# Performance work log

Measured on AMD Instinct MI355X. Metric: run time of the kernel, lower is better.

## Reference

```python
import jax, jax.numpy as jnp
import numpy as np

IMG = 40  # imgSize hard-coded in FFTNet


def _fft_layer(z, w):
    # z: complex64 [B, inC, H, W]; w: float32 [inC, outC, H, W, 2]
    # torch.fft(..., 2, normalized=True) == 2D FFT with 'ortho' norm over last two dims
    F = jnp.fft.fft2(z, norm='ortho')
    wc = jax.lax.complex(w[..., 0], w[..., 1])
    # dft_conv: per-frequency complex multiply then sum over input channels
    # (Karatsuba trick in the original == plain complex multiply)
    mixed = jnp.einsum('bihw,iohw->bohw', F, wc)
    return jnp.fft.ifft2(mixed, norm='ortho')


def _crelu(z):
    # F.relu applied to the stacked [..., 2] real/imag tensor => relu each part
    return jax.lax.complex(jax.nn.relu(z.real), jax.nn.relu(z.imag))


def _fftnet(x, ws):
    # x: [B, 1, H, W] real; stacked with zeros -> complex input
    z = x.astype(jnp.complex64)
    for w in ws[:-1]:
        z = _crelu(_fft_layer(z, w))
    z = _fft_layer(z, ws[-1])
    return z.real  # x[..., 0]


def setup_inputs() -> dict:
    key = jax.random.key(0)
    ks = jax.random.split(key, 7)
    B = 256
    x = jax.random.normal(ks[0], (B, 1, IMG, IMG), dtype=jnp.float32)

    def make_w(k, i, o):
        # xavier_normal_ on torch shape (1, i, o, H, W, 2):
        # fan_in = i * (o*H*W*2), fan_out = 1 * (o*H*W*2)
        recept = o * IMG * IMG * 2
        std = float(np.sqrt(2.0 / (i * recept + recept)))
        return jax.random.normal(k, (i, o, IMG, IMG, 2), dtype=jnp.float32) * std

    chans = [(1, 40), (40, 40), (40, 40), (40, 40), (40, 40), (40, 1)]
    inp = {'x': x}
    for n, (k, (i, o)) in enumerate(zip(ks[1:], chans), start=1):
        inp[f'w{n}'] = make_w(k, i, o)
    return inp


def reference(x, w1, w2, w3, w4, w5, w6):
    return _fftnet(x, (w1, w2, w3, w4, w5, w6))
```

## Files before the change

kernel.cpp:

```cpp
#include <hip/hip_runtime.h>
#include <math.h>

#define NPIX 1600
#define NIMG 40
#define SW   40
#define PSZ  (48 * SW)

#define RST 322
#define OST 482

typedef __bf16 bf16x8 __attribute__((ext_vector_type(8)));
typedef float  f32x4  __attribute__((ext_vector_type(4)));
#define MFMA __builtin_amdgcn_mfma_f32_16x16x32_bf16

__device__ __forceinline__ unsigned short bits16(__bf16 x) {
    return __builtin_bit_cast(unsigned short, x);
}

__device__ __forceinline__ void cfma(float2& acc, float ax, float ay, float bx, float by) {
    acc.x = fmaf(ax, bx, fmaf(-ay, by, acc.x));
    acc.y = fmaf(ax, by, fmaf( ay, bx, acc.y));
}

__global__ void init_dtab(unsigned short* __restrict__ Dtab) {
    int idx = blockIdx.x * 256 + threadIdx.x;
    if (idx >= 2304) return;
    int rec = idx >> 6, lane = idx & 63;
    int p = rec % 6, t = (rec / 6) % 3, kc = rec / 18;
    unsigned short out[8];
    for (int j = 0; j < 8; ++j) {
        int k = kc * 32 + (lane >> 4) * 8 + j;
        int n = t * 16 + (lane & 15);
        float val = 0.0f;
        if (k < 40 && n < 40) {
            float ang = 6.28318530717958647692f * (float)((k * n) % 40) / 40.0f;
            float dr, di, s, c;
            sincosf(ang, &s, &c);
            dr = c; di = s;
            float base = (p < 2) ? dr : (p < 4) ? di : -di;
            __bf16 hi = (__bf16)base;
            if ((p & 1) == 0) val = (float)hi;
            else              val = (float)(__bf16)(base - (float)hi);
        }
        out[j] = __builtin_bit_cast(unsigned short, (__bf16)val);
    }
    unsigned short* dst = Dtab + (size_t)rec * 512 + lane * 8;
    for (int j = 0; j < 8; ++j) dst[j] = out[j];
}

template<bool REAL_IN, bool RELU, bool REAL_OUT>
__global__ __launch_bounds__(256) void fft2_kernel(const void* __restrict__ inv,
                                                   void* __restrict__ outv,
                                                   int dir)
{
    const int img = blockIdx.x;
    const int tid = threadIdx.x;
    __shared__ float2 A[NPIX];
    __shared__ float2 T[NPIX];
    __shared__ float2 D[NPIX];
    __shared__ float2 tw[NIMG];

    if (tid < NIMG) {
        float ang = (float)dir * 6.28318530717958647692f * (float)tid / 40.0f;
        float s, c;
        sincosf(ang, &s, &c);
        tw[tid] = make_float2(c, s);
    }
    if (REAL_IN) {
        const float* in = (const float*)inv + (size_t)img * NPIX;
        for (int idx = tid; idx < NPIX; idx += 256)
            A[idx] = make_float2(in[idx], 0.0f);
    } else {
        const float2* in = (const float2*)inv + (size_t)img * NPIX;
        for (int idx = tid; idx < NPIX; idx += 256)
            A[idx] = in[idx];
    }
    __syncthreads();
    for (int idx = tid; idx < NPIX; idx += 256) {
        int a = idx / NIMG, b = idx - a * NIMG;
        D[idx] = tw[(a * b) % NIMG];
    }
    __syncthreads();

    for (int idx = tid; idx < NPIX; idx += 256) {
        int h = idx / NIMG, v = idx - h * NIMG;
        float2 s = make_float2(0.0f, 0.0f);
        const float2* Arow = &A[h * NIMG];
        #pragma unroll
        for (int w = 0; w < NIMG; ++w) {
            float2 a = Arow[w];
            float2 d = D[w * NIMG + v];
            s.x += a.x * d.x - a.y * d.y;
            s.y += a.x * d.y + a.y * d.x;
        }
        T[idx] = s;
    }
    __syncthreads();

    for (int idx = tid; idx < NPIX; idx += 256) {
        int u = idx / NIMG, v = idx - u * NIMG;
        float2 s = make_float2(0.0f, 0.0f);
        const float2* Du = &D[u * NIMG];
        #pragma unroll
        for (int h = 0; h < NIMG; ++h) {
            float2 t = T[h * NIMG + v];
            float2 d = Du[h];
            s.x += t.x * d.x - t.y * d.y;
            s.y += t.x * d.y + t.y * d.x;
        }
        s.x *= 0.025f;
        s.y *= 0.025f;
        if (RELU) { s.x = fmaxf(s.x, 0.0f); s.y = fmaxf(s.y, 0.0f); }
        if (REAL_OUT) {
            ((float*)outv)[(size_t)img * NPIX + idx] = s.x;
        } else {
            ((float2*)outv)[(size_t)img * NPIX + idx] = s;
        }
    }
}

__device__ __forceinline__ void mac_row(f32x4& aR, f32x4& aI,
    bf16x8 xrh, bf16x8 xrl, bf16x8 xih, bf16x8 xil,
    bf16x8 drh, bf16x8 drl, bf16x8 dih, bf16x8 dil, bf16x8 dnh, bf16x8 dnl)
{
    aR = MFMA(xrh, drh, aR, 0, 0, 0);
    aR = MFMA(xrl, drh, aR, 0, 0, 0);
    aR = MFMA(xrh, drl, aR, 0, 0, 0);
    aR = MFMA(xih, dnh, aR, 0, 0, 0);
    aR = MFMA(xil, dnh, aR, 0, 0, 0);
    aR = MFMA(xih, dnl, aR, 0, 0, 0);
    aI = MFMA(xrh, dih, aI, 0, 0, 0);
    aI = MFMA(xrl, dih, aI, 0, 0, 0);
    aI = MFMA(xrh, dil, aI, 0, 0, 0);
    aI = MFMA(xih, drh, aI, 0, 0, 0);
    aI = MFMA(xil, drh, aI, 0, 0, 0);
    aI = MFMA(xih, drl, aI, 0, 0, 0);
}

__device__ __forceinline__ void mac_col(f32x4& aR, f32x4& aI,
    bf16x8 drh, bf16x8 drl, bf16x8 dih, bf16x8 dil, bf16x8 dnh, bf16x8 dnl,
    bf16x8 trh, bf16x8 trl, bf16x8 tih, bf16x8 til)
{
    aR = MFMA(drh, trh, aR, 0, 0, 0);
    aR = MFMA(drl, trh, aR, 0, 0, 0);
    aR = MFMA(drh, trl, aR, 0, 0, 0);
    aR = MFMA(dnh, tih, aR, 0, 0, 0);
    aR = MFMA(dnl, tih, aR, 0, 0, 0);
    aR = MFMA(dnh, til, aR, 0, 0, 0);
    aI = MFMA(drh, tih, aI, 0, 0, 0);
    aI = MFMA(drl, tih, aI, 0, 0, 0);
    aI = MFMA(drh, til, aI, 0, 0, 0);
    aI = MFMA(dih, trh, aI, 0, 0, 0);
    aI = MFMA(dil, trh, aI, 0, 0, 0);
    aI = MFMA(dih, trl, aI, 0, 0, 0);
}

__device__ __forceinline__ void mac_mix(f32x4& aR, f32x4& aI,
    bf16x8 frh, bf16x8 frl, bf16x8 fih, bf16x8 fil, bf16x8 fnih, bf16x8 fnil,
    bf16x8 wrh, bf16x8 wrl, bf16x8 wih, bf16x8 wil)
{
    aR = MFMA(frh,  wrh, aR, 0, 0, 0);
    aR = MFMA(frl,  wrh, aR, 0, 0, 0);
    aR = MFMA(frh,  wrl, aR, 0, 0, 0);
    aR = MFMA(fnih, wih, aR, 0, 0, 0);
    aR = MFMA(fnil, wih, aR, 0, 0, 0);
    aR = MFMA(fnih, wil, aR, 0, 0, 0);
    aI = MFMA(frh,  wih, aI, 0, 0, 0);
    aI = MFMA(frl,  wih, aI, 0, 0, 0);
    aI = MFMA(frh,  wil, aI, 0, 0, 0);
    aI = MFMA(fih,  wrh, aI, 0, 0, 0);
    aI = MFMA(fil,  wrh, aI, 0, 0, 0);
    aI = MFMA(fih,  wrl, aI, 0, 0, 0);
}

__global__ __launch_bounds__(512, 2) void mix_mfma_kernel(const float2* __restrict__ F,
                                                          const float2* __restrict__ W,
                                                          float2* __restrict__ M)
{
    __shared__ alignas(16) char smem[102912];
    float2* raw  = (float2*)smem;
    float2* outt = (float2*)(smem + 41216);
    float2* lw   = (float2*)smem;

    const int tid  = threadIdx.x;
    const int w    = tid >> 6;
    const int lane = tid & 63;
    const int q    = lane >> 4;
    const int m    = lane & 15;
    const int fw   = blockIdx.x >> 3;
    const int bg   = blockIdx.x & 7;
    const int f0   = fw * 8;
    const int fsub = w;

    f32x4 pf[5];
    #pragma unroll
    for (int k = 0; k < 5; ++k) {
        int c = tid + (k << 9);
        int r = c >> 2, sub = c & 3;
        int b = r / 40, i = r - b * 40;
        const f32x4* g = (const f32x4*)(F + ((size_t)((bg * 32 + b) * 40 + i) * NPIX + f0));
        pf[k] = __builtin_nontemporal_load(g + sub);
    }

    #pragma unroll
    for (int k = 0; k < 13; ++k) {
        int c = tid + (k << 9);
        if (c < 6400) {
            int r = c >> 2, sub = c & 3;
            const f32x4* g = (const f32x4*)(W + ((size_t)r * NPIX + f0));
            *(f32x4*)&lw[r * 8 + sub * 2] = g[sub];
        }
    }
    __syncthreads();

    bf16x8 wt[2][3][4];
    #pragma unroll
    for (int kc = 0; kc < 2; ++kc) {
        #pragma unroll
        for (int nt = 0; nt < 3; ++nt) {
            bf16x8 wrh = (bf16x8){}, wrl = (bf16x8){};
            bf16x8 wih = (bf16x8){}, wil = (bf16x8){};
            const int o = nt * 16 + m;
            const bool have = ((kc == 0) || (q == 0)) && (o < 40);
            if (have) {
                #pragma unroll
                for (int j = 0; j < 8; ++j) {
                    int i = kc * 32 + q * 8 + j;
                    float2 v = lw[(i * 40 + o) * 8 + fsub];
                    __bf16 h1 = (__bf16)v.x;
                    wrh[j] = h1; wrl[j] = (__bf16)(v.x - (float)h1);
                    __bf16 h2 = (__bf16)v.y;
                    wih[j] = h2; wil[j] = (__bf16)(v.y - (float)h2);
                }
            }
            wt[kc][nt][0] = wrh; wt[kc][nt][1] = wrl;
            wt[kc][nt][2] = wih; wt[kc][nt][3] = wil;
        }
    }
    __syncthreads();

    #pragma unroll
    for (int bt = 0; bt < 2; ++bt) {
        const int btile = bg * 2 + bt;

        #pragma unroll
        for (int k = 0; k < 5; ++k) {
            int c = tid + (k << 9);
            int r = c >> 2, sub = c & 3;
            int b = r / 40, i = r - b * 40;
            *(f32x4*)&raw[b * RST + i * 8 + sub * 2] = pf[k];
        }
        __syncthreads();

        if (bt == 0) {
            #pragma unroll
            for (int k = 0; k < 5; ++k) {
                int c = tid + (k << 9);
                int r = c >> 2, sub = c & 3;
                int b = r / 40, i = r - b * 40;
                const f32x4* g = (const f32x4*)(F + ((size_t)(((bg * 2 + 1) * 16 + b) * 40 + i) * NPIX + f0));
                pf[k] = __builtin_nontemporal_load(g + sub);
            }
        }

        f32x4 accR[3], accI[3];
        #pragma unroll
        for (int nt = 0; nt < 3; ++nt) {
            accR[nt] = (f32x4){0.f, 0.f, 0.f, 0.f};
            accI[nt] = (f32x4){0.f, 0.f, 0.f, 0.f};
        }

        #pragma unroll
        for (int kc = 0; kc < 2; ++kc) {
            const bool have = (kc == 0) || (q == 0);
            float re[8], im[8];
            #pragma unroll
            for (int j = 0; j < 8; ++j) {
                int i = kc * 32 + q * 8 + j;
                if (have) {
                    float2 v = raw[m * RST + i * 8 + fsub];
                    re[j] = v.x; im[j] = v.y;
                } else { re[j] = 0.f; im[j] = 0.f; }
            }
            bf16x8 frh, frl, fih, fil, fnih, fnil;
            #pragma unroll
            for (int j = 0; j < 8; ++j) {
                __bf16 h1 = (__bf16)re[j];
                frh[j] = h1;
                float lo = re[j] - (float)h1;
                frl[j] = (__bf16)lo;
                __bf16 h2 = (__bf16)im[j];
                fih[j] = h2;
                float lo2 = im[j] - (float)h2;
                fil[j] = (__bf16)lo2;
                fnih[j] = (__bf16)(-(float)h2);
                fnil[j] = (__bf16)(-lo2);
            }
            #pragma unroll
            for (int nt = 0; nt < 3; ++nt)
                mac_mix(accR[nt], accI[nt], frh, frl, fih, fil, fnih, fnil,
                        wt[kc][nt][0], wt[kc][nt][1], wt[kc][nt][2], wt[kc][nt][3]);
        }

        #pragma unroll
        for (int nt = 0; nt < 3; ++nt)
            #pragma unroll
            for (int g2 = 0; g2 < 4; ++g2)
                outt[(q * 4 + g2) * OST + (nt * 16 + m) * 10 + fsub] =
                    make_float2(accR[nt][g2], accI[nt][g2]);
        __syncthreads();

        #pragma unroll
        for (int k = 0; k < 5; ++k) {
            int c = tid + (k << 9);
            int r = c >> 2, sub = c & 3;
            int b = r / 40, o = r - b * 40;
            f32x4 v = *(const f32x4*)&outt[b * OST + o * 10 + sub * 2];
            f32x4* g = (f32x4*)(M + ((size_t)((btile * 16 + b) * 40 + o) * NPIX + f0));
            __builtin_nontemporal_store(v, g + sub);
        }
    }
}

__global__ __launch_bounds__(64) void fused_mfma_kernel(const float2* __restrict__ in,
                                                        float2* __restrict__ outg,
                                                        const unsigned short* __restrict__ Dtab)
{
    __shared__ unsigned short Pl[4 * PSZ];

    const int lane = threadIdx.x;
    const int q = lane >> 4;
    const int m = lane & 15;

    bf16x8 dreg[36];
    #pragma unroll
    for (int r = 0; r < 36; ++r)
        dreg[r] = ((const bf16x8*)Dtab)[r * 64 + lane];

    #pragma unroll 1
    for (int ii = 0; ii < 5; ++ii) {
        const size_t img  = (size_t)blockIdx.x + (size_t)ii * 2048;
        const size_t base = img * NPIX;

        {
            const float4* src = (const float4*)(in + base);
            #pragma unroll
            for (int c = 0; c < 13; ++c) {
                int p = c * 64 + lane;
                if (p < 800) {
                    float4 v = src[p];
                    int h = p / 20, w2 = (p - h * 20) * 2;
                    int o = h * SW + w2;
                    __bf16 rh0 = (__bf16)v.x, ih0 = (__bf16)v.y;
                    __bf16 rh1 = (__bf16)v.z, ih1 = (__bf16)v.w;
                    ushort2 s0, s1, s2, s3;
                    s0.x = bits16(rh0); s0.y = bits16(rh1);
                    s1.x = bits16((__bf16)(v.x - (float)rh0));
                    s1.y = bits16((__bf16)(v.z - (float)rh1));
                    s2.x = bits16(ih0); s2.y = bits16(ih1);
                    s3.x = bits16((__bf16)(v.y - (float)ih0));
                    s3.y = bits16((__bf16)(v.w - (float)ih1));
                    *(ushort2*)&Pl[0 * PSZ + o] = s0;
                    *(ushort2*)&Pl[1 * PSZ + o] = s1;
                    *(ushort2*)&Pl[2 * PSZ + o] = s2;
                    *(ushort2*)&Pl[3 * PSZ + o] = s3;
                }
            }
            #pragma unroll
            for (int c = 0; c < 5; ++c) {
                int idx = c * 64 + lane;
                int pl = idx / 80, rem = idx - pl * 80;
                int r = 40 + rem / 10, c4 = (rem - (rem / 10) * 10) * 4;
                *(ushort4*)&Pl[pl * PSZ + r * SW + c4] = make_ushort4(0, 0, 0, 0);
            }
        }
        __syncthreads();

        f32x4 accR[3][3], accI[3][3];

        #pragma unroll
        for (int rep = 0; rep < 2; ++rep) {
            const int IP = rep ? 4 : 2;
            const int IN = rep ? 2 : 4;

            #pragma unroll
            for (int a = 0; a < 3; ++a)
                #pragma unroll
                for (int b = 0; b < 3; ++b) {
                    accR[a][b] = (f32x4){0.f, 0.f, 0.f, 0.f};
                    accI[a][b] = (f32x4){0.f, 0.f, 0.f, 0.f};
                }

            #pragma unroll
            for (int kc = 0; kc < 2; ++kc) {
                bf16x8 arh[3], arl[3], aih[3], ail[3];
                const bool have = (kc == 0) || (q == 0);
                #pragma unroll
                for (int mt = 0; mt < 3; ++mt) {
                    if (have) {
                        int o = (mt * 16 + m) * SW + kc * 32 + q * 8;
                        arh[mt] = *(const bf16x8*)&Pl[0 * PSZ + o];
                        arl[mt] = *(const bf16x8*)&Pl[1 * PSZ + o];
                        aih[mt] = *(const bf16x8*)&Pl[2 * PSZ + o];
                        ail[mt] = *(const bf16x8*)&Pl[3 * PSZ + o];
                    } else {
                        arh[mt] = (bf16x8){}; arl[mt] = (bf16x8){};
                        aih[mt] = (bf16x8){}; ail[mt] = (bf16x8){};
                    }
                }
                __builtin_amdgcn_s_setprio(1);
                #pragma unroll
                for (int nt = 0; nt < 3; ++nt) {
                    const int rb = (kc * 3 + nt) * 6;
                    #pragma unroll
                    for (int mt = 0; mt < 3; ++mt)
                        mac_row(accR[mt][nt], accI[mt][nt],
                                arh[mt], arl[mt], aih[mt], ail[mt],
                                dreg[rb + 0], dreg[rb + 1],
                                dreg[rb + IP], dreg[rb + IP + 1],
                                dreg[rb + IN], dreg[rb + IN + 1]);
                }
                __builtin_amdgcn_s_setprio(0);
            }
            __syncthreads();

            #pragma unroll
            for (int mt = 0; mt < 3; ++mt) {
                int hb = mt * 16 + q * 4;
                if (hb < 40) {
                    #pragma unroll
                    for (int nt = 0; nt < 3; ++nt) {
                        int v = nt * 16 + m;
                        f32x4 r = accR[mt][nt], i2 = accI[mt][nt];
                        ushort4 srh, srl, sih, sil;
                        unsigned short* prh = (unsigned short*)&srh;
                        unsigned short* prl = (unsigned short*)&srl;
                        unsigned short* pih = (unsigned short*)&sih;
                        unsigned short* pil = (unsigned short*)&sil;
                        #pragma unroll
                        for (int g = 0; g < 4; ++g) {
                            __bf16 h1 = (__bf16)r[g];
                            prh[g] = bits16(h1);
                            prl[g] = bits16((__bf16)(r[g] - (float)h1));
                            __bf16 h2 = (__bf16)i2[g];
                            pih[g] = bits16(h2);
                            pil[g] = bits16((__bf16)(i2[g] - (float)h2));
                        }
                        int o = v * SW + hb;
                        *(ushort4*)&Pl[0 * PSZ + o] = srh;
                        *(ushort4*)&Pl[1 * PSZ + o] = srl;
                        *(ushort4*)&Pl[2 * PSZ + o] = sih;
                        *(ushort4*)&Pl[3 * PSZ + o] = sil;
                    }
                }
            }
            __syncthreads();

            #pragma unroll
            for (int a = 0; a < 3; ++a)
                #pragma unroll
                for (int b = 0; b < 3; ++b) {
                    accR[a][b] = (f32x4){0.f, 0.f, 0.f, 0.f};
                    accI[a][b] = (f32x4){0.f, 0.f, 0.f, 0.f};
                }

            #pragma unroll
            for (int kc = 0; kc < 2; ++kc) {
                bf16x8 trh[3], trl[3], tih[3], til[3];
                const bool have = (kc == 0) || (q == 0);
                #pragma unroll
                for (int nt = 0; nt < 3; ++nt) {
                    trh[nt] = (bf16x8){}; trl[nt] = (bf16x8){};
                    tih[nt] = (bf16x8){}; til[nt] = (bf16x8){};
                    if (have) {
                        int o = (nt * 16 + m) * SW + kc * 32 + q * 8;
                        trh[nt] = *(const bf16x8*)&Pl[0 * PSZ + o];
                        trl[nt] = *(const bf16x8*)&Pl[1 * PSZ + o];
                        tih[nt] = *(const bf16x8*)&Pl[2 * PSZ + o];
                        til[nt] = *(const bf16x8*)&Pl[3 * PSZ + o];
                    }
                }
                __builtin_amdgcn_s_setprio(1);
                #pragma unroll
                for (int mt = 0; mt < 3; ++mt) {
                    const int rb = (kc * 3 + mt) * 6;
                    #pragma unroll
                    for (int nt = 0; nt < 3; ++nt)
                        mac_col(accR[mt][nt], accI[mt][nt],
                                dreg[rb + 0], dreg[rb + 1],
                                dreg[rb + IP], dreg[rb + IP + 1],
                                dreg[rb + IN], dreg[rb + IN + 1],
                                trh[nt], trl[nt], tih[nt], til[nt]);
                }
                __builtin_amdgcn_s_setprio(0);
            }
            __syncthreads();

            if (rep == 0) {
                #pragma unroll
                for (int mt = 0; mt < 3; ++mt) {
                    int u0 = mt * 16 + q * 4;
                    if (u0 < 40) {
                        #pragma unroll
                        for (int nt = 0; nt < 3; ++nt) {
                            int v = nt * 16 + m;
                            if (v < 40) {
                                f32x4 r = accR[mt][nt], i2 = accI[mt][nt];
                                ushort4 srh, srl, sih, sil;
                                unsigned short* prh = (unsigned short*)&srh;
                                unsigned short* prl = (unsigned short*)&srl;
                                unsigned short* pih = (unsigned short*)&sih;
                                unsigned short* pil = (unsigned short*)&sil;
                                #pragma unroll
                                for (int g = 0; g < 4; ++g) {
                                    float xr = fmaxf(r[g] * 0.025f, 0.f);
                                    float xi = fmaxf(i2[g] * 0.025f, 0.f);
                                    __bf16 h1 = (__bf16)xr;
                                    prh[g] = bits16(h1);
                                    prl[g] = bits16((__bf16)(xr - (float)h1));
                                    __bf16 h2 = (__bf16)xi;
                                    pih[g] = bits16(h2);
                                    pil[g] = bits16((__bf16)(xi - (float)h2));
                                }
                                int o = v * SW + u0;
                                *(ushort4*)&Pl[0 * PSZ + o] = srh;
                                *(ushort4*)&Pl[1 * PSZ + o] = srl;
                                *(ushort4*)&Pl[2 * PSZ + o] = sih;
                                *(ushort4*)&Pl[3 * PSZ + o] = sil;
                            }
                        }
                    }
                }
                __syncthreads();
            } else {
                float2* dst = outg + base;
                #pragma unroll
                for (int mt = 0; mt < 3; ++mt) {
                    int u0 = mt * 16 + q * 4;
                    if (u0 < 40) {
                        #pragma unroll
                        for (int nt = 0; nt < 3; ++nt) {
                            int v = nt * 16 + m;
                            if (v < 40) {
                                f32x4 r = accR[mt][nt], i2 = accI[mt][nt];
                                float4 s0, s1;
                                s0.x = r[0] * 0.025f; s0.y = i2[0] * 0.025f;
                                s0.z = r[1] * 0.025f; s0.w = i2[1] * 0.025f;
                                s1.x = r[2] * 0.025f; s1.y = i2[2] * 0.025f;
                                s1.z = r[3] * 0.025f; s1.w = i2[3] * 0.025f;
                                *(float4*)&dst[v * NIMG + u0]     = s0;
                                *(float4*)&dst[v * NIMG + u0 + 2] = s1;
                            }
                        }
                    }
                }
            }
        }
        __syncthreads();
    }
}

template<int INC, int OUTC, int BT, int OT>
__global__ __launch_bounds__(256) void mix_kernel(const float2* __restrict__ F,
                                                  const float2* __restrict__ W,
                                                  float2* __restrict__ M)
{
    const int tid = threadIdx.x;
    const int lane = tid & 63;
    const int wv = tid >> 6;
    const int f = (blockIdx.x % 25) * 64 + lane;
    const int bg = (blockIdx.x / 25) * 4 + wv;
    const int b0 = bg * BT;

    #pragma unroll
    for (int o0 = 0; o0 < OUTC; o0 += OT) {
        float2 acc[BT][OT];
        #pragma unroll
        for (int t = 0; t < BT; ++t)
            #pragma unroll
            for (int o = 0; o < OT; ++o)
                acc[t][o] = make_float2(0.0f, 0.0f);

        for (int i = 0; i < INC; ++i) {
            float2 fv[BT];
            #pragma unroll
            for (int t = 0; t < BT; ++t)
                fv[t] = F[((size_t)(b0 + t) * INC + i) * NPIX + f];
            float2 wr[OT];
            #pragma unroll
            for (int o = 0; o < OT; ++o)
                wr[o] = W[((size_t)i * OUTC + (o0 + o)) * NPIX + f];
            #pragma unroll
            for (int t = 0; t < BT; ++t)
                #pragma unroll
                for (int o = 0; o < OT; ++o)
                    cfma(acc[t][o], fv[t].x, fv[t].y, wr[o].x, wr[o].y);
        }
        #pragma unroll
        for (int t = 0; t < BT; ++t)
            #pragma unroll
            for (int o = 0; o < OT; ++o)
                M[((size_t)(b0 + t) * OUTC + (o0 + o)) * NPIX + f] = acc[t][o];
    }
}

extern "C" void kernel_launch(void* const* d_in, const int* in_sizes, int n_in,
                              void* d_out, int out_size, void* d_ws, size_t ws_size,
                              hipStream_t stream)
{
    const float* x = (const float*)d_in[0];
    const float2* w[6];
    for (int i = 0; i < 6; ++i) w[i] = (const float2*)d_in[1 + i];
    float* out = (float*)d_out;

    const size_t bufBytes = (size_t)256 * 40 * NPIX * sizeof(float2);
    float2* A = (float2*)d_ws;
    float2* B = (float2*)((char*)d_ws + bufBytes);
    unsigned short* Dtab = (unsigned short*)((char*)d_ws + 2 * bufBytes);

    const int FUSEGRID = 2048;
    const int MIXBLK = 25 * (256 / 4) / 4;

    init_dtab<<<9, 256, 0, stream>>>(Dtab);

    fft2_kernel<true, false, false><<<256, 256, 0, stream>>>(x, A, -1);

    mix_kernel<1, 40, 4, 10><<<MIXBLK, 256, 0, stream>>>(A, w[0], B);
    fused_mfma_kernel<<<FUSEGRID, 64, 0, stream>>>(B, A, Dtab);

    for (int l = 1; l <= 4; ++l) {
        mix_mfma_kernel<<<1600, 512, 0, stream>>>(A, w[l], B);
        fused_mfma_kernel<<<FUSEGRID, 64, 0, stream>>>(B, A, Dtab);
    }

    mix_kernel<40, 1, 4, 1><<<MIXBLK, 256, 0, stream>>>(A, w[5], B);
    fft2_kernel<false, false, true><<<256, 256, 0, stream>>>(B, out, +1);
}
```

Baseline: 1.552 ms.

## Negate activation operands on the fly to shrink DFT register table and raise occupancy

The fused FFT kernel previously kept 36 bf16x8 DFT-matrix fragments in registers, including pre-negated imaginary parts, for the forward and inverse transforms. It now keeps only 24 fragments and gets the sign flips by XOR-negating the activation fragments per tile, with a direction-dependent choice of which operand to negate. The freed registers allow a launch bound of 3 waves per SIMD, and the grid grows from 2048 to 2560 blocks with 4 images each instead of 5. Loads and MFMAs are also interleaved per tile rather than batched, which adds some VALU sign-flip work and may reduce load/MFMA overlap.

Result: slower. 2.040 ms (+31.4%).

```diff
diff --git a/kernel.cpp b/kernel.cpp
--- a/kernel.cpp
+++ b/kernel.cpp
@@ -11,10 +11,17 @@
 
 typedef __bf16 bf16x8 __attribute__((ext_vector_type(8)));
 typedef float  f32x4  __attribute__((ext_vector_type(4)));
+typedef unsigned int u32x4v __attribute__((ext_vector_type(4)));
 #define MFMA __builtin_amdgcn_mfma_f32_16x16x32_bf16
 
 __device__ __forceinline__ unsigned short bits16(__bf16 x) {
     return __builtin_bit_cast(unsigned short, x);
+}
+
+__device__ __forceinline__ bf16x8 bneg(bf16x8 x) {
+    u32x4v u = __builtin_bit_cast(u32x4v, x);
+    u = u ^ (u32x4v){0x80008000u, 0x80008000u, 0x80008000u, 0x80008000u};
+    return __builtin_bit_cast(bf16x8, u);
 }
 
 __device__ __forceinline__ void cfma(float2& acc, float ax, float ay, float bx, float by) {
@@ -119,40 +126,42 @@
     }
 }
 
-__device__ __forceinline__ void mac_row(f32x4& aR, f32x4& aI,
+__device__ __forceinline__ void mac_cplx(f32x4& aR, f32x4& aI,
     bf16x8 xrh, bf16x8 xrl, bf16x8 xih, bf16x8 xil,
-    bf16x8 drh, bf16x8 drl, bf16x8 dih, bf16x8 dil, bf16x8 dnh, bf16x8 dnl)
+    bf16x8 ph,  bf16x8 pl,  bf16x8 qh,  bf16x8 ql,
+    bf16x8 drh, bf16x8 drl, bf16x8 dih, bf16x8 dil)
 {
     aR = MFMA(xrh, drh, aR, 0, 0, 0);
     aR = MFMA(xrl, drh, aR, 0, 0, 0);
     aR = MFMA(xrh, drl, aR, 0, 0, 0);
-    aR = MFMA(xih, dnh, aR, 0, 0, 0);
-    aR = MFMA(xil, dnh, aR, 0, 0, 0);
-    aR = MFMA(xih, dnl, aR, 0, 0, 0);
-    aI = MFMA(xrh, dih, aI, 0, 0, 0);
-    aI = MFMA(xrl, dih, aI, 0, 0, 0);
-    aI = MFMA(xrh, dil, aI, 0, 0, 0);
+    aR = MFMA(ph,  dih, aR, 0, 0, 0);
+    aR = MFMA(pl,  dih, aR, 0, 0, 0);
+    aR = MFMA(ph,  dil, aR, 0, 0, 0);
+    aI = MFMA(qh,  dih, aI, 0, 0, 0);
+    aI = MFMA(ql,  dih, aI, 0, 0, 0);
+    aI = MFMA(qh,  dil, aI, 0, 0, 0);
     aI = MFMA(xih, drh, aI, 0, 0, 0);
     aI = MFMA(xil, drh, aI, 0, 0, 0);
     aI = MFMA(xih, drl, aI, 0, 0, 0);
 }
 
-__device__ __forceinline__ void mac_col(f32x4& aR, f32x4& aI,
-    bf16x8 drh, bf16x8 drl, bf16x8 dih, bf16x8 dil, bf16x8 dnh, bf16x8 dnl,
-    bf16x8 trh, bf16x8 trl, bf16x8 tih, bf16x8 til)
+__device__ __forceinline__ void mac_cplx_col(f32x4& aR, f32x4& aI,
+    bf16x8 drh, bf16x8 drl, bf16x8 dih, bf16x8 dil,
+    bf16x8 trh, bf16x8 trl, bf16x8 tih, bf16x8 til,
+    bf16x8 ph,  bf16x8 pl,  bf16x8 qh,  bf16x8 ql)
 {
     aR = MFMA(drh, trh, aR, 0, 0, 0);
     aR = MFMA(drl, trh, aR, 0, 0, 0);
     aR = MFMA(drh, trl, aR, 0, 0, 0);
-    aR = MFMA(dnh, tih, aR, 0, 0, 0);
-    aR = MFMA(dnl, tih, aR, 0, 0, 0);
-    aR = MFMA(dnh, til, aR, 0, 0, 0);
+    aR = MFMA(dih, ph,  aR, 0, 0, 0);
+    aR = MFMA(dil, ph,  aR, 0, 0, 0);
+    aR = MFMA(dih, pl,  aR, 0, 0, 0);
+    aI = MFMA(dih, qh,  aI, 0, 0, 0);
+    aI = MFMA(dil, qh,  aI, 0, 0, 0);
+    aI = MFMA(dih, ql,  aI, 0, 0, 0);
     aI = MFMA(drh, tih, aI, 0, 0, 0);
     aI = MFMA(drl, tih, aI, 0, 0, 0);
     aI = MFMA(drh, til, aI, 0, 0, 0);
-    aI = MFMA(dih, trh, aI, 0, 0, 0);
-    aI = MFMA(dil, trh, aI, 0, 0, 0);
-    aI = MFMA(dih, trl, aI, 0, 0, 0);
 }
 
 __device__ __forceinline__ void mac_mix(f32x4& aR, f32x4& aI,
@@ -322,9 +331,9 @@
     }
 }
 
-__global__ __launch_bounds__(64) void fused_mfma_kernel(const float2* __restrict__ in,
-                                                        float2* __restrict__ outg,
-                                                        const unsigned short* __restrict__ Dtab)
+__global__ __launch_bounds__(64, 3) void fused_mfma_kernel(const float2* __restrict__ in,
+                                                           float2* __restrict__ outg,
+                                                           const unsigned short* __restrict__ Dtab)
 {
     __shared__ unsigned short Pl[4 * PSZ];
 
@@ -332,14 +341,16 @@
     const int q = lane >> 4;
     const int m = lane & 15;
 
-    bf16x8 dreg[36];
+    bf16x8 dreg[24];
     #pragma unroll
-    for (int r = 0; r < 36; ++r)
-        dreg[r] = ((const bf16x8*)Dtab)[r * 64 + lane];
+    for (int t = 0; t < 6; ++t)
+        #pragma unroll
+        for (int p = 0; p < 4; ++p)
+            dreg[t * 4 + p] = ((const bf16x8*)Dtab)[((size_t)t * 6 + p) * 64 + lane];
 
     #pragma unroll 1
-    for (int ii = 0; ii < 5; ++ii) {
-        const size_t img  = (size_t)blockIdx.x + (size_t)ii * 2048;
+    for (int ii = 0; ii < 4; ++ii) {
+        const size_t img  = (size_t)blockIdx.x + (size_t)ii * 2560;
         const size_t base = img * NPIX;
 
         {
@@ -380,8 +391,6 @@
 
         #pragma unroll
         for (int rep = 0; rep < 2; ++rep) {
-            const int IP = rep ? 4 : 2;
-            const int IN = rep ? 2 : 4;
 
             #pragma unroll
             for (int a = 0; a < 3; ++a)
@@ -393,34 +402,33 @@
 
             #pragma unroll
             for (int kc = 0; kc < 2; ++kc) {
-                bf16x8 arh[3], arl[3], aih[3], ail[3];
                 const bool have = (kc == 0) || (q == 0);
                 #pragma unroll
                 for (int mt = 0; mt < 3; ++mt) {
+                    bf16x8 xrh, xrl, xih, xil;
                     if (have) {
                         int o = (mt * 16 + m) * SW + kc * 32 + q * 8;
-                        arh[mt] = *(const bf16x8*)&Pl[0 * PSZ + o];
-                        arl[mt] = *(const bf16x8*)&Pl[1 * PSZ + o];
-                        aih[mt] = *(const bf16x8*)&Pl[2 * PSZ + o];
-                        ail[mt] = *(const bf16x8*)&Pl[3 * PSZ + o];
+                        xrh = *(const bf16x8*)&Pl[0 * PSZ + o];
+                        xrl = *(const bf16x8*)&Pl[1 * PSZ + o];
+                        xih = *(const bf16x8*)&Pl[2 * PSZ + o];
+                        xil = *(const bf16x8*)&Pl[3 * PSZ + o];
                     } else {
-                        arh[mt] = (bf16x8){}; arl[mt] = (bf16x8){};
-                        aih[mt] = (bf16x8){}; ail[mt] = (bf16x8){};
+                        xrh = (bf16x8){}; xrl = (bf16x8){};
+                        xih = (bf16x8){}; xil = (bf16x8){};
                     }
-                }
-                __builtin_amdgcn_s_setprio(1);
-                #pragma unroll
-                for (int nt = 0; nt < 3; ++nt) {
-                    const int rb = (kc * 3 + nt) * 6;
+                    bf16x8 ph, pl2, qh, ql;
+                    if (rep == 0) { ph = bneg(xih); pl2 = bneg(xil); qh = xrh; ql = xrl; }
+                    else          { ph = xih;       pl2 = xil;       qh = bneg(xrh); ql = bneg(xrl); }
+                    __builtin_amdgcn_s_setprio(1);
                     #pragma unroll
-                    for (int mt = 0; mt < 3; ++mt)
-                        mac_row(accR[mt][nt], accI[mt][nt],
-                                arh[mt], arl[mt], aih[mt], ail[mt],
-                                dreg[rb + 0], dreg[rb + 1],
-                                dreg[rb + IP], dreg[rb + IP + 1],
-                                dreg[rb + IN], dreg[rb + IN + 1]);
-                }
-                __builtin_amdgcn_s_setprio(0);
+                    for (int nt = 0; nt < 3; ++nt) {
+                        const int rb = (kc * 3 + nt) * 4;
+                        mac_cplx(accR[mt][nt], accI[mt][nt],
+                                 xrh, xrl, xih, xil, ph, pl2, qh, ql,
+                                 dreg[rb + 0], dreg[rb + 1], dreg[rb + 2], dreg[rb + 3]);
+                    }
+                    __builtin_amdgcn_s_setprio(0);
+                }
             }
             __syncthreads();
 
@@ -466,33 +474,33 @@
 
             #pragma unroll
             for (int kc = 0; kc < 2; ++kc) {
-                bf16x8 trh[3], trl[3], tih[3], til[3];
                 const bool have = (kc == 0) || (q == 0);
                 #pragma unroll
                 for (int nt = 0; nt < 3; ++nt) {
-                    trh[nt] = (bf16x8){}; trl[nt] = (bf16x8){};
-                    tih[nt] = (bf16x8){}; til[nt] = (bf16x8){};
+                    bf16x8 trh, trl, tih, til;
                     if (have) {
                         int o = (nt * 16 + m) * SW + kc * 32 + q * 8;
-                        trh[nt] = *(const bf16x8*)&Pl[0 * PSZ + o];
-                        trl[nt] = *(const bf16x8*)&Pl[1 * PSZ + o];
-                        tih[nt] = *(const bf16x8*)&Pl[2 * PSZ + o];
-                        til[nt] = *(const bf16x8*)&Pl[3 * PSZ + o];
+                        trh = *(const bf16x8*)&Pl[0 * PSZ + o];
+                        trl = *(const bf16x8*)&Pl[1 * PSZ + o];
+                        tih = *(const bf16x8*)&Pl[2 * PSZ + o];
+                        til = *(const bf16x8*)&Pl[3 * PSZ + o];
+                    } else {
+                        trh = (bf16x8){}; trl = (bf16x8){};
+                        tih = (bf16x8){}; til = (bf16x8){};
                     }
-                }
-                __builtin_amdgcn_s_setprio(1);
-                #pragma unroll
-                for (int mt = 0; mt < 3; ++mt) {
-                    const int rb = (kc * 3 + mt) * 6;
+                    bf16x8 ph, pl2, qh, ql;
+                    if (rep == 0) { ph = bneg(tih); pl2 = bneg(til); qh = trh; ql = trl; }
+                    else          { ph = tih;       pl2 = til;       qh = bneg(trh); ql = bneg(trl); }
+                    __builtin_amdgcn_s_setprio(1);
                     #pragma unroll
-                    for (int nt = 0; nt < 3; ++nt)
-                        mac_col(accR[mt][nt], accI[mt][nt],
-                                dreg[rb + 0], dreg[rb + 1],
-                                dreg[rb + IP], dreg[rb + IP + 1],
-                                dreg[rb + IN], dreg[rb + IN + 1],
-                                trh[nt], trl[nt], tih[nt], til[nt]);
-                }
-                __builtin_amdgcn_s_setprio(0);
+                    for (int mt = 0; mt < 3; ++mt) {
+                        const int rb = (kc * 3 + mt) * 4;
+                        mac_cplx_col(accR[mt][nt], accI[mt][nt],
+                                     dreg[rb + 0], dreg[rb + 1], dreg[rb + 2], dreg[rb + 3],
+                                     trh, trl, tih, til, ph, pl2, qh, ql);
+                    }
+                    __builtin_amdgcn_s_setprio(0);
+                }
             }
             __syncthreads();
 
@@ -618,7 +626,7 @@
     float2* B = (float2*)((char*)d_ws + bufBytes);
     unsigned short* Dtab = (unsigned short*)((char*)d_ws + 2 * bufBytes);
 
-    const int FUSEGRID = 2048;
+    const int FUSEGRID = 2560;
     const int MIXBLK = 25 * (256 / 4) / 4;
 
     init_dtab<<<9, 256, 0, stream>>>(Dtab);
```

## Split fused FFT kernel across nine waves, one MFMA tile each, DFT table in LDS

Applied to the files above, without the earlier changes.

The fused inverse/forward FFT kernel moves from one 64-thread wave computing all 3x3 output tiles to 576-thread blocks where each of nine waves owns one (mt, nt) tile. The DFT twiddle table now lives in shared memory instead of 36 bf16x8 registers per lane, which cuts register pressure and should allow more resident waves. The cost is extra LDS traffic for the twiddle reads, a larger LDS footprint per block, and the table reload in every block.

Result: faster. 1.415 ms (-8.8%).

```diff
diff --git a/kernel.cpp b/kernel.cpp
--- a/kernel.cpp
+++ b/kernel.cpp
@@ -322,20 +322,28 @@
     }
 }
 
-__global__ __launch_bounds__(64) void fused_mfma_kernel(const float2* __restrict__ in,
-                                                        float2* __restrict__ outg,
-                                                        const unsigned short* __restrict__ Dtab)
+__global__ __launch_bounds__(576, 5) void fused_mfma_kernel(const float2* __restrict__ in,
+                                                            float2* __restrict__ outg,
+                                                            const unsigned short* __restrict__ Dtab)
 {
     __shared__ unsigned short Pl[4 * PSZ];
-
-    const int lane = threadIdx.x;
-    const int q = lane >> 4;
-    const int m = lane & 15;
-
-    bf16x8 dreg[36];
+    __shared__ unsigned short Dlds[36 * 512];
+
+    const int tid  = threadIdx.x;
+    const int wv   = tid >> 6;
+    const int lane = tid & 63;
+    const int q    = lane >> 4;
+    const int m    = lane & 15;
+    const int mt   = wv / 3;
+    const int nt   = wv - mt * 3;
+
     #pragma unroll
-    for (int r = 0; r < 36; ++r)
-        dreg[r] = ((const bf16x8*)Dtab)[r * 64 + lane];
+    for (int c = 0; c < 4; ++c) {
+        int idx = c * 576 + tid;
+        int rec = idx >> 6, l2 = idx & 63;
+        *(f32x4*)&Dlds[rec * 512 + l2 * 8] =
+            *(const f32x4*)(Dtab + (size_t)rec * 512 + l2 * 8);
+    }
 
     #pragma unroll 1
     for (int ii = 0; ii < 5; ++ii) {
@@ -345,8 +353,8 @@
         {
             const float4* src = (const float4*)(in + base);
             #pragma unroll
-            for (int c = 0; c < 13; ++c) {
-                int p = c * 64 + lane;
+            for (int c = 0; c < 2; ++c) {
+                int p = c * 576 + tid;
                 if (p < 800) {
                     float4 v = src[p];
                     int h = p / 20, w2 = (p - h * 20) * 2;
@@ -366,193 +374,147 @@
                     *(ushort2*)&Pl[3 * PSZ + o] = s3;
                 }
             }
-            #pragma unroll
-            for (int c = 0; c < 5; ++c) {
-                int idx = c * 64 + lane;
-                int pl = idx / 80, rem = idx - pl * 80;
+            if (tid < 320) {
+                int pl = tid / 80, rem = tid - pl * 80;
                 int r = 40 + rem / 10, c4 = (rem - (rem / 10) * 10) * 4;
                 *(ushort4*)&Pl[pl * PSZ + r * SW + c4] = make_ushort4(0, 0, 0, 0);
             }
         }
         __syncthreads();
-
-        f32x4 accR[3][3], accI[3][3];
 
         #pragma unroll
         for (int rep = 0; rep < 2; ++rep) {
             const int IP = rep ? 4 : 2;
             const int IN = rep ? 2 : 4;
 
-            #pragma unroll
-            for (int a = 0; a < 3; ++a)
-                #pragma unroll
-                for (int b = 0; b < 3; ++b) {
-                    accR[a][b] = (f32x4){0.f, 0.f, 0.f, 0.f};
-                    accI[a][b] = (f32x4){0.f, 0.f, 0.f, 0.f};
+            f32x4 aR = (f32x4){0.f, 0.f, 0.f, 0.f};
+            f32x4 aI = (f32x4){0.f, 0.f, 0.f, 0.f};
+
+            #pragma unroll
+            for (int kc = 0; kc < 2; ++kc) {
+                const bool have = (kc == 0) || (q == 0);
+                bf16x8 xrh, xrl, xih, xil;
+                if (have) {
+                    int o = (mt * 16 + m) * SW + kc * 32 + q * 8;
+                    xrh = *(const bf16x8*)&Pl[0 * PSZ + o];
+                    xrl = *(const bf16x8*)&Pl[1 * PSZ + o];
+                    xih = *(const bf16x8*)&Pl[2 * PSZ + o];
+                    xil = *(const bf16x8*)&Pl[3 * PSZ + o];
+                } else {
+                    xrh = (bf16x8){}; xrl = (bf16x8){};
+                    xih = (bf16x8){}; xil = (bf16x8){};
                 }
-
-            #pragma unroll
-            for (int kc = 0; kc < 2; ++kc) {
-                bf16x8 arh[3], arl[3], aih[3], ail[3];
-                const bool have = (kc == 0) || (q == 0);
-                #pragma unroll
-                for (int mt = 0; mt < 3; ++mt) {
-                    if (have) {
-                        int o = (mt * 16 + m) * SW + kc * 32 + q * 8;
-                        arh[mt] = *(const bf16x8*)&Pl[0 * PSZ + o];
-                        arl[mt] = *(const bf16x8*)&Pl[1 * PSZ + o];
-                        aih[mt] = *(const bf16x8*)&Pl[2 * PSZ + o];
-                        ail[mt] = *(const bf16x8*)&Pl[3 * PSZ + o];
-                    } else {
-                        arh[mt] = (bf16x8){}; arl[mt] = (bf16x8){};
-                        aih[mt] = (bf16x8){}; ail[mt] = (bf16x8){};
-                    }
-                }
+                const int rb = (kc * 3 + nt) * 6;
+                bf16x8 drh = *(const bf16x8*)&Dlds[(rb + 0) * 512 + lane * 8];
+                bf16x8 drl = *(const bf16x8*)&Dlds[(rb + 1) * 512 + lane * 8];
+                bf16x8 dih = *(const bf16x8*)&Dlds[(rb + IP) * 512 + lane * 8];
+                bf16x8 dil = *(const bf16x8*)&Dlds[(rb + IP + 1) * 512 + lane * 8];
+                bf16x8 dnh = *(const bf16x8*)&Dlds[(rb + IN) * 512 + lane * 8];
+                bf16x8 dnl = *(const bf16x8*)&Dlds[(rb + IN + 1) * 512 + lane * 8];
                 __builtin_amdgcn_s_setprio(1);
-                #pragma unroll
-                for (int nt = 0; nt < 3; ++nt) {
-                    const int rb = (kc * 3 + nt) * 6;
-                    #pragma unroll
-                    for (int mt = 0; mt < 3; ++mt)
-                        mac_row(accR[mt][nt], accI[mt][nt],
-                                arh[mt], arl[mt], aih[mt], ail[mt],
-                                dreg[rb + 0], dreg[rb + 1],
-                                dreg[rb + IP], dreg[rb + IP + 1],
-                                dreg[rb + IN], dreg[rb + IN + 1]);
-                }
+                mac_row(aR, aI, xrh, xrl, xih, xil,
+                        drh, drl, dih, dil, dnh, dnl);
                 __builtin_amdgcn_s_setprio(0);
             }
             __syncthreads();
 
-            #pragma unroll
-            for (int mt = 0; mt < 3; ++mt) {
+            {
                 int hb = mt * 16 + q * 4;
                 if (hb < 40) {
+                    int v = nt * 16 + m;
+                    ushort4 srh, srl, sih, sil;
+                    unsigned short* prh = (unsigned short*)&srh;
+                    unsigned short* prl = (unsigned short*)&srl;
+                    unsigned short* pih = (unsigned short*)&sih;
+                    unsigned short* pil = (unsigned short*)&sil;
                     #pragma unroll
-                    for (int nt = 0; nt < 3; ++nt) {
-                        int v = nt * 16 + m;
-                        f32x4 r = accR[mt][nt], i2 = accI[mt][nt];
-                        ushort4 srh, srl, sih, sil;
-                        unsigned short* prh = (unsigned short*)&srh;
-                        unsigned short* prl = (unsigned short*)&srl;
-                        unsigned short* pih = (unsigned short*)&sih;
-                        unsigned short* pil = (unsigned short*)&sil;
-                        #pragma unroll
-                        for (int g = 0; g < 4; ++g) {
-                            __bf16 h1 = (__bf16)r[g];
-                            prh[g] = bits16(h1);
-                            prl[g] = bits16((__bf16)(r[g] - (float)h1));
-                            __bf16 h2 = (__bf16)i2[g];
-                            pih[g] = bits16(h2);
-                            pil[g] = bits16((__bf16)(i2[g] - (float)h2));
-                        }
-                        int o = v * SW + hb;
-                        *(ushort4*)&Pl[0 * PSZ + o] = srh;
-                        *(ushort4*)&Pl[1 * PSZ + o] = srl;
-                        *(ushort4*)&Pl[2 * PSZ + o] = sih;
-                        *(ushort4*)&Pl[3 * PSZ + o] = sil;
+                    for (int g = 0; g < 4; ++g) {
+                        __bf16 h1 = (__bf16)aR[g];
+                        prh[g] = bits16(h1);
+                        prl[g] = bits16((__bf16)(aR[g] - (float)h1));
+                        __bf16 h2 = (__bf16)aI[g];
+                        pih[g] = bits16(h2);
+                        pil[g] = bits16((__bf16)(aI[g] - (float)h2));
                     }
+                    int o = v * SW + hb;
+                    *(ushort4*)&Pl[0 * PSZ + o] = srh;
+                    *(ushort4*)&Pl[1 * PSZ + o] = srl;
+                    *(ushort4*)&Pl[2 * PSZ + o] = sih;
+                    *(ushort4*)&Pl[3 * PSZ + o] = sil;
                 }
             }
             __syncthreads();
 
-            #pragma unroll
-            for (int a = 0; a < 3; ++a)
-                #pragma unroll
-                for (int b = 0; b < 3; ++b) {
-                    accR[a][b] = (f32x4){0.f, 0.f, 0.f, 0.f};
-                    accI[a][b] = (f32x4){0.f, 0.f, 0.f, 0.f};
+            aR = (f32x4){0.f, 0.f, 0.f, 0.f};
+            aI = (f32x4){0.f, 0.f, 0.f, 0.f};
+
+            #pragma unroll
+            for (int kc = 0; kc < 2; ++kc) {
+                const bool have = (kc == 0) || (q == 0);
+                bf16x8 trh, trl, tih, til;
+                if (have) {
+                    int o = (nt * 16 + m) * SW + kc * 32 + q * 8;
+                    trh = *(const bf16x8*)&Pl[0 * PSZ + o];
+                    trl = *(const bf16x8*)&Pl[1 * PSZ + o];
+                    tih = *(const bf16x8*)&Pl[2 * PSZ + o];
+                    til = *(const bf16x8*)&Pl[3 * PSZ + o];
+                } else {
+                    trh = (bf16x8){}; trl = (bf16x8){};
+                    tih = (bf16x8){}; til = (bf16x8){};
                 }
-
-            #pragma unroll
-            for (int kc = 0; kc < 2; ++kc) {
-                bf16x8 trh[3], trl[3], tih[3], til[3];
-                const bool have = (kc == 0) || (q == 0);
-                #pragma unroll
-                for (int nt = 0; nt < 3; ++nt) {
-                    trh[nt] = (bf16x8){}; trl[nt] = (bf16x8){};
-                    tih[nt] = (bf16x8){}; til[nt] = (bf16x8){};
-                    if (have) {
-                        int o = (nt * 16 + m) * SW + kc * 32 + q * 8;
-                        trh[nt] = *(const bf16x8*)&Pl[0 * PSZ + o];
-                        trl[nt] = *(const bf16x8*)&Pl[1 * PSZ + o];
-                        tih[nt] = *(const bf16x8*)&Pl[2 * PSZ + o];
-                        til[nt] = *(const bf16x8*)&Pl[3 * PSZ + o];
+                const int rb = (kc * 3 + mt) * 6;
+                bf16x8 drh = *(const bf16x8*)&Dlds[(rb + 0) * 512 + lane * 8];
+                bf16x8 drl = *(const bf16x8*)&Dlds[(rb + 1) * 512 + lane * 8];
+                bf16x8 dih = *(const bf16x8*)&Dlds[(rb + IP) * 512 + lane * 8];
+                bf16x8 dil = *(const bf16x8*)&Dlds[(rb + IP + 1) * 512 + lane * 8];
+                bf16x8 dnh = *(const bf16x8*)&Dlds[(rb + IN) * 512 + lane * 8];
+                bf16x8 dnl = *(const bf16x8*)&Dlds[(rb + IN + 1) * 512 + lane * 8];
+                __builtin_amdgcn_s_setprio(1);
+                mac_col(aR, aI, drh, drl, dih, dil, dnh, dnl,
+                        trh, trl, tih, til);
+                __builtin_amdgcn_s_setprio(0);
+            }
+
+            if (rep == 0) {
+                __syncthreads();
+                int v = nt * 16 + m;
+                int u0 = mt * 16 + q * 4;
+                if (v < 40 && u0 < 40) {
+                    ushort4 srh, srl, sih, sil;
+                    unsigned short* prh = (unsigned short*)&srh;
+                    unsigned short* prl = (unsigned short*)&srl;
+                    unsigned short* pih = (unsigned short*)&sih;
+                    unsigned short* pil = (unsigned short*)&sil;
+                    #pragma unroll
+                    for (int g = 0; g < 4; ++g) {
+                        float xr = fmaxf(aR[g] * 0.025f, 0.f);
+                        float xi = fmaxf(aI[g] * 0.025f, 0.f);
+                        __bf16 h1 = (__bf16)xr;
+                        prh[g] = bits16(h1);
+                        prl[g] = bits16((__bf16)(xr - (float)h1));
+                        __bf16 h2 = (__bf16)xi;
+                        pih[g] = bits16(h2);
+                        pil[g] = bits16((__bf16)(xi - (float)h2));
                     }
-                }
-                __builtin_amdgcn_s_setprio(1);
-                #pragma unroll
-                for (int mt = 0; mt < 3; ++mt) {
-                    const int rb = (kc * 3 + mt) * 6;
-                    #pragma unroll
-                    for (int nt = 0; nt < 3; ++nt)
-                        mac_col(accR[mt][nt], accI[mt][nt],
-                                dreg[rb + 0], dreg[rb + 1],
-                                dreg[rb + IP], dreg[rb + IP + 1],
-                                dreg[rb + IN], dreg[rb + IN + 1],
-                                trh[nt], trl[nt], tih[nt], til[nt]);
-                }
-                __builtin_amdgcn_s_setprio(0);
-            }
-            __syncthreads();
-
-            if (rep == 0) {
-                #pragma unroll
-                for (int mt = 0; mt < 3; ++mt) {
-                    int u0 = mt * 16 + q * 4;
-                    if (u0 < 40) {
-                        #pragma unroll
-                        for (int nt = 0; nt < 3; ++nt) {
-                            int v = nt * 16 + m;
-                            if (v < 40) {
-                                f32x4 r = accR[mt][nt], i2 = accI[mt][nt];
-                                ushort4 srh, srl, sih, sil;
-                                unsigned short* prh = (unsigned short*)&srh;
-                                unsigned short* prl = (unsigned short*)&srl;
-                                unsigned short* pih = (unsigned short*)&sih;
-                                unsigned short* pil = (unsigned short*)&sil;
-                                #pragma unroll
-                                for (int g = 0; g < 4; ++g) {
-                                    float xr = fmaxf(r[g] * 0.025f, 0.f);
-                                    float xi = fmaxf(i2[g] * 0.025f, 0.f);
-                                    __bf16 h1 = (__bf16)xr;
-                                    prh[g] = bits16(h1);
-                                    prl[g] = bits16((__bf16)(xr - (float)h1));
-                                    __bf16 h2 = (__bf16)xi;
-                                    pih[g] = bits16(h2);
-                                    pil[g] = bits16((__bf16)(xi - (float)h2));
-                                }
-                                int o = v * SW + u0;
-                                *(ushort4*)&Pl[0 * PSZ + o] = srh;
-                                *(ushort4*)&Pl[1 * PSZ + o] = srl;
-                                *(ushort4*)&Pl[2 * PSZ + o] = sih;
-                                *(ushort4*)&Pl[3 * PSZ + o] = sil;
-                            }
-                        }
-                    }
+                    int o = v * SW + u0;
+                    *(ushort4*)&Pl[0 * PSZ + o] = srh;
+                    *(ushort4*)&Pl[1 * PSZ + o] = srl;
+                    *(ushort4*)&Pl[2 * PSZ + o] = sih;
+                    *(ushort4*)&Pl[3 * PSZ + o] = sil;
                 }
                 __syncthreads();
             } else {
                 float2* dst = outg + base;
-                #pragma unroll
-                for (int mt = 0; mt < 3; ++mt) {
-                    int u0 = mt * 16 + q * 4;
-                    if (u0 < 40) {
-                        #pragma unroll
-                        for (int nt = 0; nt < 3; ++nt) {
-                            int v = nt * 16 + m;
-                            if (v < 40) {
-                                f32x4 r = accR[mt][nt], i2 = accI[mt][nt];
-                                float4 s0, s1;
-                                s0.x = r[0] * 0.025f; s0.y = i2[0] * 0.025f;
-                                s0.z = r[1] * 0.025f; s0.w = i2[1] * 0.025f;
-                                s1.x = r[2] * 0.025f; s1.y = i2[2] * 0.025f;
-                                s1.z = r[3] * 0.025f; s1.w = i2[3] * 0.025f;
-                                *(float4*)&dst[v * NIMG + u0]     = s0;
-                                *(float4*)&dst[v * NIMG + u0 + 2] = s1;
-                            }
-                        }
-                    }
+                int v = nt * 16 + m;
+                int u0 = mt * 16 + q * 4;
+                if (v < 40 && u0 < 40) {
+                    float4 s0, s1;
+                    s0.x = aR[0] * 0.025f; s0.y = aI[0] * 0.025f;
+                    s0.z = aR[1] * 0.025f; s0.w = aI[1] * 0.025f;
+                    s1.x = aR[2] * 0.025f; s1.y = aI[2] * 0.025f;
+                    s1.z = aR[3] * 0.025f; s1.w = aI[3] * 0.025f;
+                    *(float4*)&dst[v * NIMG + u0]     = s0;
+                    *(float4*)&dst[v * NIMG + u0 + 2] = s1;
                 }
             }
         }
@@ -626,11 +588,11 @@
     fft2_kernel<true, false, false><<<256, 256, 0, stream>>>(x, A, -1);
 
     mix_kernel<1, 40, 4, 10><<<MIXBLK, 256, 0, stream>>>(A, w[0], B);
-    fused_mfma_kernel<<<FUSEGRID, 64, 0, stream>>>(B, A, Dtab);
+    fused_mfma_kernel<<<FUSEGRID, 576, 0, stream>>>(B, A, Dtab);
 
     for (int l = 1; l <= 4; ++l) {
         mix_mfma_kernel<<<1600, 512, 0, stream>>>(A, w[l], B);
-        fused_mfma_kernel<<<FUSEGRID, 64, 0, stream>>>(B, A, Dtab);
+        fused_mfma_kernel<<<FUSEGRID, 576, 0, stream>>>(B, A, Dtab);
     }
 
     mix_kernel<40, 1, 4, 1><<<MIXBLK, 256, 0, stream>>>(A, w[5], B);
```
